# Optimization experiments

Measured on AMD Instinct MI355X. Metric: run time of the kernel, lower is better.

Reference implementation:

```python
import jax, jax.numpy as jnp
import numpy as np

# --- model/problem constants (match init_kwargs) ---
B = 1024      # batch
F = 512       # featureSize
H = 1024      # hiddenSize
S = 8         # symmetrySize
BOX = 12      # boxSize
MAXB = 64     # maxBoxes
MAXSY = 64    # maxSyms
MAXS = 16     # max stack depth (pattern uses <= 2)
L = 126


def setup_inputs() -> dict:
    key = jax.random.key(0)
    ks = jax.random.split(key, 9)

    def lin(k, out_d, in_d):
        k1, k2 = jax.random.split(k)
        bound = 1.0 / np.sqrt(in_d)
        W = jax.random.uniform(k1, (out_d, in_d), minval=-bound, maxval=bound, dtype=jnp.float32)
        b = jax.random.uniform(k2, (out_d,), minval=-bound, maxval=bound, dtype=jnp.float32)
        return W, b

    Wd, bd = lin(ks[0], H, F)      # AdjDecoder.decode
    Wl, bl = lin(ks[1], F, H)      # AdjDecoder.left
    Wr, br = lin(ks[2], F, H)      # AdjDecoder.right
    Wsd, bsd = lin(ks[3], H, F)    # SymDecoder.decode
    Wsf, bsf = lin(ks[4], F, H)    # SymDecoder.left
    Wss, bss = lin(ks[5], S, H)    # SymDecoder.right
    Wbox, bbox = lin(ks[6], BOX, F)  # BoxDecoder.decode

    inputStacks = jax.random.normal(ks[7], (B, F), dtype=jnp.float32)

    # Valid stack program, PROCESSING order: [adj, sym, box] * 42.
    # stack depth: 1 ->(1) 2 ->(2) 2 ->(0) 1 ; 42 boxes, 42 syms.
    proc = np.tile(np.array([1, 2, 0], dtype=np.int32), L // 3)
    stored = proc[::-1].copy()  # forward() processes operations in reverse
    operations = jnp.asarray(np.tile(stored[None, None, :], (B, 1, 1)))  # [B,1,L]

    return {"inputStacks": inputStacks, "operations": operations,
            "Wd": Wd, "bd": bd, "Wl": Wl, "bl": bl, "Wr": Wr, "br": br,
            "Wsd": Wsd, "bsd": bsd, "Wsf": Wsf, "bsf": bsf, "Wss": Wss, "bss": bss,
            "Wbox": Wbox, "bbox": bbox}


def _forward(inputStacks, operations, Wd, bd, Wl, bl, Wr, br,
             Wsd, bsd, Wsf, bsf, Wss, bss, Wbox, bbox):
    Bn, Fn = inputStacks.shape
    ops_proc = jnp.flip(operations[:, 0, :], axis=1).T  # [L, B] processing order

    stack = jnp.zeros((Bn, MAXS, Fn), inputStacks.dtype).at[:, 0, :].set(inputStacks)
    sp = jnp.ones((Bn,), jnp.int32)           # stack pointer (size)
    boxbuf = jnp.zeros((Bn, MAXB, Fn), inputStacks.dtype)
    bc = jnp.zeros((Bn,), jnp.int32)
    symbuf = jnp.zeros((Bn, MAXSY, S), inputStacks.dtype)
    sc = jnp.zeros((Bn,), jnp.int32)
    rows = jnp.arange(Bn)

    def step(carry, op):
        stack, sp, boxbuf, bc, symbuf, sc = carry
        top_idx = jnp.clip(sp - 1, 0, MAXS - 1)
        top = stack[rows, top_idx]                      # [B,F]
        # AdjDecoder on every sample (selected by op==1)
        h = jnp.tanh(top @ Wd.T + bd)
        l = jnp.tanh(h @ Wl.T + bl)
        r = jnp.tanh(h @ Wr.T + br)
        # SymDecoder on every sample (selected by op==2)
        hs = jnp.tanh(top @ Wsd.T + bsd)
        f = jnp.tanh(hs @ Wsf.T + bsf)
        s = jnp.tanh(hs @ Wss.T + bss)

        is0 = op == 0
        is1 = op == 1
        is2 = op == 2
        # value replacing the popped top (for op 1 -> left, op 2 -> folded)
        val_top = jnp.where(is1[:, None], l, jnp.where(is2[:, None], f, top))
        pos = jnp.arange(MAXS)[None, :]
        m_top = (pos == top_idx[:, None]) & (~is0)[:, None]
        m_r = (pos == jnp.clip(sp, 0, MAXS - 1)[:, None]) & is1[:, None]
        stack = jnp.where(m_r[..., None], r[:, None, :],
                          jnp.where(m_top[..., None], val_top[:, None, :], stack))
        posb = jnp.arange(MAXB)[None, :]
        mb = (posb == bc[:, None]) & is0[:, None]
        boxbuf = jnp.where(mb[..., None], top[:, None, :], boxbuf)
        poss = jnp.arange(MAXSY)[None, :]
        ms = (poss == sc[:, None]) & is2[:, None]
        symbuf = jnp.where(ms[..., None], s[:, None, :], symbuf)

        sp = sp + jnp.where(is0, -1, jnp.where(is1, 1, 0)).astype(sp.dtype)
        bc = bc + is0.astype(bc.dtype)
        sc = sc + is2.astype(sc.dtype)
        return (stack, sp, boxbuf, bc, symbuf, sc), None

    (stack, sp, boxbuf, bc, symbuf, sc), _ = jax.lax.scan(
        step, (stack, sp, boxbuf, bc, symbuf, sc), ops_proc)

    # boxStacks[i].reverse(); boxDecoder; pad with zeros to maxBoxes
    jb = jnp.arange(MAXB)
    bidx = bc[:, None] - 1 - jb[None, :]          # reversed order
    bvalid = bidx >= 0
    bfeat = jnp.take_along_axis(boxbuf, jnp.clip(bidx, 0, MAXB - 1)[..., None], axis=1)
    boxes = jnp.tanh(bfeat @ Wbox.T + bbox) * bvalid[..., None].astype(bfeat.dtype)

    js = jnp.arange(MAXSY)
    sidx = sc[:, None] - 1 - js[None, :]
    svalid = sidx >= 0
    syms = jnp.take_along_axis(symbuf, jnp.clip(sidx, 0, MAXSY - 1)[..., None], axis=1)
    syms = syms * svalid[..., None].astype(syms.dtype)

    return boxes, syms  # [B, MAXB, BOX], [B, MAXSY, S]


def reference(inputStacks, operations, Wd, bd, Wl, bl, Wr, br,
              Wsd, bsd, Wsf, bsf, Wss, bss, Wbox, bbox):
    return _forward(inputStacks, operations, Wd, bd, Wl, bl, Wr, br,
                    Wsd, bsd, Wsf, bsf, Wss, bss, Wbox, bbox)
```

## Files before the change

kernel.cpp:

```cpp
#include <hip/hip_runtime.h>
#include <stdint.h>

#define B_     1024
#define F_     512
#define H_     1024
#define S_     8
#define BOX_   12
#define MAXB_  64
#define MAXSY_ 64
#define L_     126
#define STK_   3
#define NCYC_  42

typedef unsigned short u16;
typedef unsigned int   u32;
typedef unsigned long long u64;
typedef __attribute__((ext_vector_type(8))) short sh8;
typedef __attribute__((ext_vector_type(4))) int   i4;
typedef __attribute__((ext_vector_type(4))) float f4;

#define MFMA16(a,b,c) __builtin_amdgcn_mfma_f32_16x16x32_bf16((a),(b),(c),0,0,0)

#define XCC_ID_IMM (((32 - 1) << 11) | (0 << 6) | 20)

constexpr size_t PL_HF = (size_t)H_ * F_ * 2;
constexpr size_t PL_FH = (size_t)F_ * H_ * 2;
constexpr size_t PL_SS = 16384;
constexpr size_t PL_BX = 16384;
constexpr size_t O_WdHi  = 4096;
constexpr size_t O_WdLo  = O_WdHi  + PL_HF;
constexpr size_t O_WsdHi = O_WdLo  + PL_HF;
constexpr size_t O_WsdLo = O_WsdHi + PL_HF;
constexpr size_t O_WlHi  = O_WsdLo + PL_HF;
constexpr size_t O_WlLo  = O_WlHi  + PL_FH;
constexpr size_t O_WrHi  = O_WlLo  + PL_FH;
constexpr size_t O_WrLo  = O_WrHi  + PL_FH;
constexpr size_t O_WsfHi = O_WrLo  + PL_FH;
constexpr size_t O_WsfLo = O_WsfHi + PL_FH;
constexpr size_t O_WssHi = O_WsfLo + PL_FH;
constexpr size_t O_WssLo = O_WssHi + PL_SS;
constexpr size_t O_WbxHi = O_WssLo + PL_SS;
constexpr size_t O_WbxLo = O_WbxHi + PL_BX;
constexpr size_t SZ_STK  = (size_t)B_ * STK_ * F_ * 2;
constexpr size_t O_SHi   = O_WbxLo + PL_BX;
constexpr size_t O_SLo   = O_SHi   + SZ_STK;
constexpr size_t SZ_H    = (size_t)B_ * H_ * 2;
constexpr size_t O_HAHi  = O_SLo   + SZ_STK;
constexpr size_t O_HALo  = O_HAHi  + SZ_H;
constexpr size_t O_HSHi  = O_HALo  + SZ_H;
constexpr size_t O_HSLo  = O_HSHi  + SZ_H;
constexpr size_t SZ_FB   = (size_t)B_ * 512 * 2;
constexpr size_t O_FB0Hi = O_HSLo  + SZ_H;
constexpr size_t O_FB0Lo = O_FB0Hi + SZ_FB;
constexpr size_t O_FB1Hi = O_FB0Lo + SZ_FB;
constexpr size_t O_FB1Lo = O_FB1Hi + SZ_FB;
constexpr size_t WS_NEED = O_FB1Lo + SZ_FB;
constexpr size_t O_FLAG  = 2048;
constexpr size_t O_GFAIL = 2176;
constexpr size_t O_GXCD  = 2304;

__device__ __forceinline__ float bf2float(u16 h) {
    union { u32 u; float f; } v; v.u = ((u32)h) << 16; return v.f;
}
__device__ __forceinline__ u16 bfhi_of(float f) {
    union { float f; u32 u; } v; v.f = f;
    u32 u = v.u;
    return (u16)((u + 0x7fffu + ((u >> 16) & 1u)) >> 16);
}
__device__ __forceinline__ void split2(float x, u16& hi, u16& lo) {
    hi = bfhi_of(x);
    lo = bfhi_of(x - bf2float(hi));
}

template<bool DC>
__device__ __forceinline__ void cst(u16* p, u16 v) {
    if (DC) asm volatile("global_store_short %0, %1, off sc0 sc1"
                         :: "v"(p), "v"((u32)v) : "memory");
    else    asm volatile("global_store_short %0, %1, off"
                         :: "v"(p), "v"((u32)v) : "memory");
}
__device__ __forceinline__ void vdrain() {
    asm volatile("s_waitcnt vmcnt(0)" ::: "memory");
}

__device__ __forceinline__ void cld8(i4& d0, i4& d1, i4& d2, i4& d3,
                                     i4& d4, i4& d5, i4& d6, i4& d7,
    const u16* p0, const u16* p1, const u16* p2, const u16* p3,
    const u16* p4, const u16* p5, const u16* p6, const u16* p7)
{
    asm volatile(
        "global_load_dwordx4 %0, %8, off sc0\n\t"
        "global_load_dwordx4 %1, %9, off sc0\n\t"
        "global_load_dwordx4 %2, %10, off sc0\n\t"
        "global_load_dwordx4 %3, %11, off sc0\n\t"
        "global_load_dwordx4 %4, %12, off sc0\n\t"
        "global_load_dwordx4 %5, %13, off sc0\n\t"
        "global_load_dwordx4 %6, %14, off sc0\n\t"
        "global_load_dwordx4 %7, %15, off sc0\n\t"
        "s_waitcnt vmcnt(0)"
        : "=&v"(d0),"=&v"(d1),"=&v"(d2),"=&v"(d3),
          "=&v"(d4),"=&v"(d5),"=&v"(d6),"=&v"(d7)
        : "v"(p0),"v"(p1),"v"(p2),"v"(p3),"v"(p4),"v"(p5),"v"(p6),"v"(p7));
}

__device__ void split_range(const float* __restrict__ s, u16* hi, u16* lo,
                            int n, int t0, int stride) {
    for (int i = t0; i < n; i += stride) {
        float v = s[i];
        u16 h = bfhi_of(v);
        hi[i] = h;
        lo[i] = bfhi_of(v - bf2float(h));
    }
}

__global__ void grass_prep(const float* __restrict__ X, const int* __restrict__ ops,
                           const float* __restrict__ Wd, const float* __restrict__ Wl,
                           const float* __restrict__ Wr, const float* __restrict__ Wsd,
                           const float* __restrict__ Wsf, const float* __restrict__ Wss,
                           const float* __restrict__ Wbox, char* __restrict__ ws)
{
    const int t0 = blockIdx.x * blockDim.x + threadIdx.x;
    const int st = gridDim.x * blockDim.x;
    split_range(Wd,  (u16*)(ws + O_WdHi),  (u16*)(ws + O_WdLo),  H_ * F_, t0, st);
    split_range(Wsd, (u16*)(ws + O_WsdHi), (u16*)(ws + O_WsdLo), H_ * F_, t0, st);
    split_range(Wl,  (u16*)(ws + O_WlHi),  (u16*)(ws + O_WlLo),  F_ * H_, t0, st);
    split_range(Wr,  (u16*)(ws + O_WrHi),  (u16*)(ws + O_WrLo),  F_ * H_, t0, st);
    split_range(Wsf, (u16*)(ws + O_WsfHi), (u16*)(ws + O_WsfLo), F_ * H_, t0, st);
    split_range(Wss, (u16*)(ws + O_WssHi), (u16*)(ws + O_WssLo), S_ * H_, t0, st);
    split_range(Wbox,(u16*)(ws + O_WbxHi), (u16*)(ws + O_WbxLo), BOX_ * F_, t0, st);
    u16* SHi = (u16*)(ws + O_SHi);
    u16* SLo = (u16*)(ws + O_SLo);
    for (int i = t0; i < B_ * F_; i += st) {
        int e = i >> 9, k = i & (F_ - 1);
        float v = X[i];
        u16 h = bfhi_of(v);
        size_t off = (size_t)e * STK_ * F_ + k;
        SHi[off] = h;
        SLo[off] = bfhi_of(v - bf2float(h));
    }
    int* flag = (int*)(ws + O_FLAG);
    for (int i = t0; i < B_ * L_; i += st) {
        int t = i % L_;
        int tm = t % 3;
        int expect = (tm == 0) ? 0 : ((tm == 1) ? 2 : 1);
        if (ops[i] != expect) {
            __hip_atomic_store(flag, 1, __ATOMIC_RELAXED, __HIP_MEMORY_SCOPE_AGENT);
            break;
        }
    }
}

__device__ __forceinline__ void gbar(int* bar, int target) {
    vdrain();
    __syncthreads();
    if (threadIdx.x == 0) {
        __hip_atomic_fetch_add(bar, 1, __ATOMIC_RELAXED, __HIP_MEMORY_SCOPE_AGENT);
        while (__hip_atomic_load(bar, __ATOMIC_RELAXED, __HIP_MEMORY_SCOPE_AGENT) < target)
            __builtin_amdgcn_s_sleep(2);
    }
    __syncthreads();
}
__device__ __forceinline__ void gwait(int* ctr, int target) {
    if (threadIdx.x == 0) {
        while (__hip_atomic_load(ctr, __ATOMIC_RELAXED, __HIP_MEMORY_SCOPE_AGENT) < target)
            __builtin_amdgcn_s_sleep(2);
    }
    __syncthreads();
}

__device__ __forceinline__ void stageA_c(u16* __restrict__ lds,
    const u16* __restrict__ AHi, const u16* __restrict__ ALo,
    const int* __restrict__ aOff, int kbase, int tid)
{
    const int wv = tid >> 6, lane = tid & 63;
    const int kk = kbase + lane * 8;
    int off[16];
#pragma unroll
    for (int i = 0; i < 16; ++i) off[i] = aOff[i * 4 + wv] + kk;
    const int lx = lane * 8;
#pragma unroll
    for (int half = 0; half < 2; ++half) {
        const u16* A = half ? ALo : AHi;
        u16* L = lds + (half ? 32768 : 0);
#pragma unroll
        for (int b = 0; b < 2; ++b) {
            const int i0 = b * 8;
            i4 d0,d1,d2,d3,d4,d5,d6,d7;
            cld8(d0,d1,d2,d3,d4,d5,d6,d7,
                 A+off[i0+0], A+off[i0+1], A+off[i0+2], A+off[i0+3],
                 A+off[i0+4], A+off[i0+5], A+off[i0+6], A+off[i0+7]);
#define STO(ii, dv) { const int m = (i0 + ii) * 4 + wv; \
                      *(i4*)(L + m * 512 + (lx ^ ((m & 7) << 3))) = dv; }
            STO(0,d0) STO(1,d1) STO(2,d2) STO(3,d3)
            STO(4,d4) STO(5,d5) STO(6,d6) STO(7,d7)
#undef STO
        }
    }
}

__device__ __forceinline__ void stageA_dc(u16* __restrict__ lds,
    const u16* __restrict__ AHi, const u16* __restrict__ ALo,
    const int* __restrict__ aOff, int kbase, int tid)
{
    const int wv = tid >> 6, lane = tid & 63;
    const int kk = kbase + lane * 8;
    int off[16];
#pragma unroll
    for (int i = 0; i < 16; ++i) off[i] = aOff[i * 4 + wv] + kk;
    u64 v[64];
#pragma unroll
    for (int i = 0; i < 16; ++i) {
        const u64* s = (const u64*)(AHi + off[i]);
        v[2 * i]     = __hip_atomic_load(s,     __ATOMIC_RELAXED, __HIP_MEMORY_SCOPE_AGENT);
        v[2 * i + 1] = __hip_atomic_load(s + 1, __ATOMIC_RELAXED, __HIP_MEMORY_SCOPE_AGENT);
    }
#pragma unroll
    for (int i = 0; i < 16; ++i) {
        const u64* s = (const u64*)(ALo + off[i]);
        v[32 + 2 * i] = __hip_atomic_load(s,     __ATOMIC_RELAXED, __HIP_MEMORY_SCOPE_AGENT);
        v[33 + 2 * i] = __hip_atomic_load(s + 1, __ATOMIC_RELAXED, __HIP_MEMORY_SCOPE_AGENT);
    }
#pragma unroll
    for (int i = 0; i < 16; ++i) {
        const int m = i * 4 + wv;
        u16* d = lds + m * 512 + ((lane * 8) ^ ((m & 7) << 3));
        ((u64*)d)[0] = v[2 * i];
        ((u64*)d)[1] = v[2 * i + 1];
        u64* d2 = (u64*)(d + 32768);
        d2[0] = v[32 + 2 * i];
        d2[1] = v[33 + 2 * i];
    }
}

__device__ __forceinline__ void kloop64(const u16* __restrict__ lds,
    const u16* __restrict__ WHi, const u16* __restrict__ WLo,
    int nRow0, int Kw, int kofs, f4 c[2][2], int lane, int wv4)
{
    const int quad = lane >> 4, mr = lane & 15;
    const int mh = wv4 & 1, nh = (wv4 >> 1) & 1;
    const int m0 = (mh * 2) * 16 + mr, m1 = m0 + 16;
    const int n0 = nRow0 + (nh * 2) * 16 + mr, n1 = n0 + 16;
    const u16* b0h = WHi + (size_t)n0 * Kw + kofs;
    const u16* b1h = WHi + (size_t)n1 * Kw + kofs;
    const u16* b0l = WLo + (size_t)n0 * Kw + kofs;
    const u16* b1l = WLo + (size_t)n1 * Kw + kofs;
    const int sw = (m0 & 7) << 3;
    const u16* A0h = lds + m0 * 512;
    const u16* A1h = lds + m1 * 512;
#pragma unroll 2
    for (int kb = 0; kb < 512; kb += 64) {
        const int k0 = kb + quad * 8, k1 = k0 + 32;
        const int x0 = k0 ^ sw, x1 = k1 ^ sw;
        sh8 B0H0 = *(const sh8*)(b0h + k0), B1H0 = *(const sh8*)(b1h + k0);
        sh8 B0L0 = *(const sh8*)(b0l + k0), B1L0 = *(const sh8*)(b1l + k0);
        sh8 B0H1 = *(const sh8*)(b0h + k1), B1H1 = *(const sh8*)(b1h + k1);
        sh8 B0L1 = *(const sh8*)(b0l + k1), B1L1 = *(const sh8*)(b1l + k1);
        sh8 A0H0 = *(const sh8*)(A0h + x0);
        sh8 A1H0 = *(const sh8*)(A1h + x0);
        sh8 A0L0 = *(const sh8*)(A0h + 32768 + x0);
        sh8 A1L0 = *(const sh8*)(A1h + 32768 + x0);
        sh8 A0H1 = *(const sh8*)(A0h + x1);
        sh8 A1H1 = *(const sh8*)(A1h + x1);
        sh8 A0L1 = *(const sh8*)(A0h + 32768 + x1);
        sh8 A1L1 = *(const sh8*)(A1h + 32768 + x1);
        c[0][0]=MFMA16(A0H0,B0H0,c[0][0]); c[0][1]=MFMA16(A0H0,B1H0,c[0][1]);
        c[1][0]=MFMA16(A1H0,B0H0,c[1][0]); c[1][1]=MFMA16(A1H0,B1H0,c[1][1]);
        c[0][0]=MFMA16(A0H0,B0L0,c[0][0]); c[0][1]=MFMA16(A0H0,B1L0,c[0][1]);
        c[1][0]=MFMA16(A1H0,B0L0,c[1][0]); c[1][1]=MFMA16(A1H0,B1L0,c[1][1]);
        c[0][0]=MFMA16(A0L0,B0H0,c[0][0]); c[0][1]=MFMA16(A0L0,B1H0,c[0][1]);
        c[1][0]=MFMA16(A1L0,B0H0,c[1][0]); c[1][1]=MFMA16(A1L0,B1H0,c[1][1]);
        c[0][0]=MFMA16(A0H1,B0H1,c[0][0]); c[0][1]=MFMA16(A0H1,B1H1,c[0][1]);
        c[1][0]=MFMA16(A1H1,B0H1,c[1][0]); c[1][1]=MFMA16(A1H1,B1H1,c[1][1]);
        c[0][0]=MFMA16(A0H1,B0L1,c[0][0]); c[0][1]=MFMA16(A0H1,B1L1,c[0][1]);
        c[1][0]=MFMA16(A1H1,B0L1,c[1][0]); c[1][1]=MFMA16(A1H1,B1L1,c[1][1]);
        c[0][0]=MFMA16(A0L1,B0H1,c[0][0]); c[0][1]=MFMA16(A0L1,B1H1,c[0][1]);
        c[1][0]=MFMA16(A1L1,B0H1,c[1][0]); c[1][1]=MFMA16(A1L1,B1H1,c[1][1]);
    }
}

__device__ __forceinline__ void kloop16(const u16* __restrict__ lds,
    const u16* __restrict__ WHi, const u16* __restrict__ WLo,
    int nValid, int Kw, int kofs, f4& c, int lane, int wv)
{
    const int quad = lane >> 4, mr = lane & 15;
    const int m = wv * 16 + mr;
    const int sm = (m & 7) << 3;
    const u16* Am = lds + m * 512;
    const bool nb = (mr < nValid);
    const u16* bh = WHi + (size_t)mr * Kw + kofs;
    const u16* bl = WLo + (size_t)mr * Kw + kofs;
#pragma unroll 2
    for (int kb = 0; kb < 512; kb += 64) {
        const int k0 = kb + quad * 8, k1 = k0 + 32;
        const int x0 = k0 ^ sm, x1 = k1 ^ sm;
        sh8 bH0 = {0,0,0,0,0,0,0,0}, bL0 = {0,0,0,0,0,0,0,0};
        sh8 bH1 = {0,0,0,0,0,0,0,0}, bL1 = {0,0,0,0,0,0,0,0};
        if (nb) {
            bH0 = *(const sh8*)(bh + k0); bL0 = *(const sh8*)(bl + k0);
            bH1 = *(const sh8*)(bh + k1); bL1 = *(const sh8*)(bl + k1);
        }
        sh8 aH0 = *(const sh8*)(Am + x0);
        sh8 aL0 = *(const sh8*)(Am + 32768 + x0);
        sh8 aH1 = *(const sh8*)(Am + x1);
        sh8 aL1 = *(const sh8*)(Am + 32768 + x1);
        c = MFMA16(aH0, bH0, c);
        c = MFMA16(aH0, bL0, c);
        c = MFMA16(aL0, bH0, c);
        c = MFMA16(aH1, bH1, c);
        c = MFMA16(aH1, bL1, c);
        c = MFMA16(aL1, bH1, c);
    }
}

__device__ __forceinline__ void zacc(f4 c[2][2]) {
    f4 z = {0.f, 0.f, 0.f, 0.f};
    c[0][0] = z; c[0][1] = z; c[1][0] = z; c[1][1] = z;
}

__device__ __forceinline__ void gemmK(u16* __restrict__ Ab,
    const u16* __restrict__ AHi, const u16* __restrict__ ALo, const int* __restrict__ aOff,
    const u16* __restrict__ WHi, const u16* __restrict__ WLo, int nRow0, int Kw,
    f4 c[2][2], int tid, int lane, int wv)
{
    zacc(c);
    for (int h = 0; h < Kw; h += 512) {
        __syncthreads();
        stageA_dc(Ab, AHi, ALo, aOff, h, tid);
        __syncthreads();
        kloop64(Ab, WHi, WLo, nRow0, Kw, h, c, lane, wv);
    }
}
__device__ __forceinline__ void gemmK16(u16* __restrict__ Ab,
    const u16* __restrict__ AHi, const u16* __restrict__ ALo, const int* __restrict__ aOff,
    const u16* __restrict__ WHi, const u16* __restrict__ WLo, int nValid, int Kw,
    f4& c, int tid, int lane, int wv)
{
    f4 z = {0.f, 0.f, 0.f, 0.f};
    c = z;
    for (int h = 0; h < Kw; h += 512) {
        __syncthreads();
        stageA_dc(Ab, AHi, ALo, aOff, h, tid);
        __syncthreads();
        kloop16(Ab, WHi, WLo, nValid, Kw, h, c, tid & 63, tid >> 6);
    }
}

__device__ __forceinline__ void pipe_gemm128(u16* __restrict__ Ab,
    const u16* __restrict__ AHi, const u16* __restrict__ ALo, const int* __restrict__ aOff,
    const u16* __restrict__ WHi, const u16* __restrict__ WLo, int col0, int Kw,
    f4 cA[2][2], f4 cB[2][2], int tid, int lane, int wv)
{
    zacc(cA); zacc(cB);
    for (int h = 0; h < Kw; h += 512) {
        __syncthreads();
        stageA_c(Ab, AHi, ALo, aOff, h, tid);
        __syncthreads();
        kloop64(Ab, WHi, WLo, col0,      Kw, h, cA, lane, wv);
        kloop64(Ab, WHi, WLo, col0 + 64, Kw, h, cB, lane, wv);
    }
}

template<bool DC>
__device__ __forceinline__ void ep_h(const f4 c[2][2], const float* __restrict__ bias,
                                     int colBase, int e0, u16* DHi, u16* DLo,
                                     int lane, int wv4)
{
    const int quad = lane >> 4, mr = lane & 15;
    const int mh = wv4 & 1, nh = (wv4 >> 1) & 1;
#pragma unroll
    for (int mi = 0; mi < 2; ++mi)
#pragma unroll
    for (int ni = 0; ni < 2; ++ni)
#pragma unroll
    for (int r = 0; r < 4; ++r) {
        int mm = (mh * 2 + mi) * 16 + quad * 4 + r;
        int nn = (nh * 2 + ni) * 16 + mr;
        float v = tanhf(c[mi][ni][r] + bias[colBase + nn]);
        u16 hi, lo; split2(v, hi, lo);
        size_t off = (size_t)(e0 + mm) * H_ + colBase + nn;
        cst<DC>(DHi + off, hi);
        cst<DC>(DLo + off, lo);
    }
}

template<bool DC>
__device__ __forceinline__ void ep_slot(const f4 c[2][2], const float* __restrict__ bias,
                                        int colBase, int slot, int e0,
                                        u16* SHi, u16* SLo, int lane, int wv4)
{
    const int quad = lane >> 4, mr = lane & 15;
    const int mh = wv4 & 1, nh = (wv4 >> 1) & 1;
#pragma unroll
    for (int mi = 0; mi < 2; ++mi)
#pragma unroll
    for (int ni = 0; ni < 2; ++ni)
#pragma unroll
    for (int r = 0; r < 4; ++r) {
        int mm = (mh * 2 + mi) * 16 + quad * 4 + r;
        int nn = (nh * 2 + ni) * 16 + mr;
        float v = tanhf(c[mi][ni][r] + bias[colBase + nn]);
        u16 hi, lo; split2(v, hi, lo);
        size_t off = ((size_t)(e0 + mm) * STK_ + slot) * F_ + colBase + nn;
        cst<DC>(SHi + off, hi);
        cst<DC>(SLo + off, lo);
    }
}

template<bool DC>
__device__ __forceinline__ void ep_fb(const f4 c[2][2], const float* __restrict__ bias,
                                      int colBase, int e0, u16* FHi, u16* FLo,
                                      int lane, int wv4)
{
    const int quad = lane >> 4, mr = lane & 15;
    const int mh = wv4 & 1, nh = (wv4 >> 1) & 1;
#pragma unroll
    for (int mi = 0; mi < 2; ++mi)
#pragma unroll
    for (int ni = 0; ni < 2; ++ni)
#pragma unroll
    for (int r = 0; r < 4; ++r) {
        int mm = (mh * 2 + mi) * 16 + quad * 4 + r;
        int nn = (nh * 2 + ni) * 16 + mr;
        float v = tanhf(c[mi][ni][r] + bias[colBase + nn]);
        u16 hi, lo; split2(v, hi, lo);
        size_t off = (size_t)(e0 + mm) * 512 + colBase + nn;
        cst<DC>(FHi + off, hi);
        cst<DC>(FLo + off, lo);
    }
}

template<bool DC>
__device__ __forceinline__ void ep_stack(const f4 c[2][2], const float* __restrict__ bias,
                                         int colBase, int opSel, bool useRi, int tix, int e0,
                                         const unsigned char* opsL, const int* spA,
                                         u16* SHi, u16* SLo, int lane, int wv)
{
    const int quad = lane >> 4, mr = lane & 15;
    const int mh = wv & 1, nh = (wv >> 1) & 1;
#pragma unroll
    for (int mi = 0; mi < 2; ++mi)
#pragma unroll
    for (int ni = 0; ni < 2; ++ni)
#pragma unroll
    for (int r = 0; r < 4; ++r) {
        int mm = (mh * 2 + mi) * 16 + quad * 4 + r;
        int nn = (nh * 2 + ni) * 16 + mr;
        if (opsL[mm * L_ + tix] != opSel) continue;
        int sp = spA[mm];
        int slot = useRi ? sp : sp - 1;
        slot = slot < 0 ? 0 : (slot > STK_ - 1 ? STK_ - 1 : slot);
        float v = tanhf(c[mi][ni][r] + bias[colBase + nn]);
        u16 hi, lo; split2(v, hi, lo);
        size_t off = ((size_t)(e0 + mm) * STK_ + slot) * F_ + colBase + nn;
        cst<DC>(SHi + off, hi);
        cst<DC>(SLo + off, lo);
    }
}

__device__ __forceinline__ void ep_small(const f4& c, const float* __restrict__ bias,
                                         int nValid, int opSel, int tix, int e0,
                                         const unsigned char* opsL, const int* eCnt, const int* eTot,
                                         float* __restrict__ outBase, int rowStride, int ncols,
                                         int lane, int wv)
{
    const int nn = lane & 15;
    if (nn >= nValid) return;
#pragma unroll
    for (int r = 0; r < 4; ++r) {
        int mm = wv * 16 + (lane >> 4) * 4 + r;
        if (opsL[mm * L_ + tix] != opSel) continue;
        int slot = eTot[mm] - 1 - eCnt[mm];
        if (slot < 0 || slot >= 64) continue;
        float v = tanhf(c[r] + bias[nn]);
        outBase[(size_t)(e0 + mm) * rowStride + slot * ncols + nn] = v;
    }
}

__device__ __forceinline__ void ep_small_u(const f4& c, const float* __restrict__ bias,
                                           int nValid, int slot, int e0,
                                           float* __restrict__ outBase, int rowStride, int ncols,
                                           int lane, int wv)
{
    const int nn = lane & 15;
    if (nn >= nValid) return;
#pragma unroll
    for (int r = 0; r < 4; ++r) {
        int mm = wv * 16 + (lane >> 4) * 4 + r;
        outBase[(size_t)(e0 + mm) * rowStride + slot * ncols + nn] = tanhf(c[r] + bias[nn]);
    }
}

__global__ __launch_bounds__(256, 1) void grass_pipe(
    const float* __restrict__ bd, const float* __restrict__ bl, const float* __restrict__ br,
    const float* __restrict__ bsd, const float* __restrict__ bsf, const float* __restrict__ bss,
    const float* __restrict__ bbox,
    char* __restrict__ ws, float* __restrict__ out)
{
    if (__hip_atomic_load((int*)(ws + O_FLAG), __ATOMIC_RELAXED, __HIP_MEMORY_SCOPE_AGENT))
        return;

    const int tid  = threadIdx.x;
    const int lane = tid & 63, wv = tid >> 6;
    const int j    = blockIdx.x >> 4;
    const int gid  = blockIdx.x & 15;
    const int e0   = gid * 64;

    const u16* WdHi  = (const u16*)(ws + O_WdHi);
    const u16* WdLo  = (const u16*)(ws + O_WdLo);
    const u16* WsdHi = (const u16*)(ws + O_WsdHi);
    const u16* WsdLo = (const u16*)(ws + O_WsdLo);
    const u16* WlHi  = (const u16*)(ws + O_WlHi);
    const u16* WlLo  = (const u16*)(ws + O_WlLo);
    const u16* WrHi  = (const u16*)(ws + O_WrHi);
    const u16* WrLo  = (const u16*)(ws + O_WrLo);
    const u16* WsfHi = (const u16*)(ws + O_WsfHi);
    const u16* WsfLo = (const u16*)(ws + O_WsfLo);
    const u16* WssHi = (const u16*)(ws + O_WssHi);
    const u16* WssLo = (const u16*)(ws + O_WssLo);
    const u16* WbxHi = (const u16*)(ws + O_WbxHi);
    const u16* WbxLo = (const u16*)(ws + O_WbxLo);
    u16* SHi  = (u16*)(ws + O_SHi);
    u16* SLo  = (u16*)(ws + O_SLo);
    u16* HAHi = (u16*)(ws + O_HAHi);
    u16* HALo = (u16*)(ws + O_HALo);
    u16* HSHi = (u16*)(ws + O_HSHi);
    u16* HSLo = (u16*)(ws + O_HSLo);
    u16* FB0Hi = (u16*)(ws + O_FB0Hi);
    u16* FB0Lo = (u16*)(ws + O_FB0Lo);
    u16* FB1Hi = (u16*)(ws + O_FB1Hi);
    u16* FB1Lo = (u16*)(ws + O_FB1Lo);
    int* cbar = (int*)ws + gid * 32;
    int* sbar = cbar + 1;
    int* pbar = cbar + 3;
    int* gx   = (int*)(ws + O_GXCD) + gid * 16;
    int* gf   = (int*)(ws + O_GFAIL) + gid;

    float* outB = out;
    float* outS = out + (size_t)B_ * MAXB_ * BOX_;

    __shared__ __align__(16) u16 Abuf[2 * 64 * 512];
    __shared__ int aS0[64], aR1[64], aR2[64], aHH[64], aFB[64];

    if (tid < 64) {
        aS0[tid] = ((e0 + tid) * STK_ + 0) * F_;
        aR1[tid] = ((e0 + tid) * STK_ + 1) * F_;
        aR2[tid] = ((e0 + tid) * STK_ + 2) * F_;
        aHH[tid] = (e0 + tid) * H_;
        aFB[tid] = (e0 + tid) * 512;
    }

    const int myxcd = (int)(__builtin_amdgcn_s_getreg(XCC_ID_IMM) & 0xf);
    if (tid == 0)
        __hip_atomic_store(gx + j, myxcd, __ATOMIC_RELAXED, __HIP_MEMORY_SCOPE_AGENT);
    gbar(pbar, 16);
    if (tid < 16) {
        int ox = __hip_atomic_load(gx + tid, __ATOMIC_RELAXED, __HIP_MEMORY_SCOPE_AGENT);
        if (ox != myxcd)
            __hip_atomic_store(gf, 1, __ATOMIC_RELAXED, __HIP_MEMORY_SCOPE_AGENT);
    }
    gbar(pbar, 32);
    if (__hip_atomic_load(gf, __ATOMIC_RELAXED, __HIP_MEMORY_SCOPE_AGENT))
        return;

    f4 cA[2][2], cB[2][2];
    f4 cs;

    if (j < 8) {
        for (int cyc = 0; cyc < NCYC_; ++cyc) {
            pipe_gemm128(Abuf, SHi, SLo, aS0, WdHi, WdLo, j * 128, F_, cA, cB, tid, lane, wv);
            ep_h<false>(cA, bd, j * 128,      e0, HAHi, HALo, lane, wv);
            ep_h<false>(cB, bd, j * 128 + 64, e0, HAHi, HALo, lane, wv);
            gbar(cbar, 8 * (2 * cyc + 1));
            if (j < 4) {
                pipe_gemm128(Abuf, HAHi, HALo, aHH, WlHi, WlLo, j * 128, H_, cA, cB, tid, lane, wv);
                ep_slot<false>(cA, bl, j * 128,      0, e0, SHi, SLo, lane, wv);
                ep_slot<false>(cB, bl, j * 128 + 64, 0, e0, SHi, SLo, lane, wv);
            } else {
                const int rs = 1 + (cyc & 1);
                pipe_gemm128(Abuf, HAHi, HALo, aHH, WrHi, WrLo, (j - 4) * 128, H_, cA, cB, tid, lane, wv);
                if (cyc >= 2) gwait(sbar, 8 * (2 * (cyc - 2) + 1));
                ep_slot<false>(cA, br, (j - 4) * 128,      rs, e0, SHi, SLo, lane, wv);
                ep_slot<false>(cB, br, (j - 4) * 128 + 64, rs, e0, SHi, SLo, lane, wv);
            }
            gbar(cbar, 8 * (2 * cyc + 2));
        }
    } else {
        const int role = j - 8;
        for (int cyc = 0; cyc < NCYC_; ++cyc) {
            gwait(cbar, 8 * (2 * cyc + 2));
            const int* aR = (cyc & 1) ? aR2 : aR1;
            pipe_gemm128(Abuf, SHi, SLo, aR, WsdHi, WsdLo, role * 128, F_, cA, cB, tid, lane, wv);
            ep_h<false>(cA, bsd, role * 128,      e0, HSHi, HSLo, lane, wv);
            ep_h<false>(cB, bsd, role * 128 + 64, e0, HSHi, HSLo, lane, wv);
            gbar(sbar, 8 * (2 * cyc + 1));
            if (role < 4) {
                u16* FH = (cyc & 1) ? FB1Hi : FB0Hi;
                u16* FL = (cyc & 1) ? FB1Lo : FB0Lo;
                pipe_gemm128(Abuf, HSHi, HSLo, aHH, WsfHi, WsfLo, role * 128, H_, cA, cB, tid, lane, wv);
                ep_fb<false>(cA, bsf, role * 128,      e0, FH, FL, lane, wv);
                ep_fb<false>(cB, bsf, role * 128 + 64, e0, FH, FL, lane, wv);
            } else if (role == 4) {
                f4 z = {0.f, 0.f, 0.f, 0.f}; cs = z;
                for (int h = 0; h < H_; h += 512) {
                    __syncthreads();
                    stageA_c(Abuf, HSHi, HSLo, aHH, h, tid);
                    __syncthreads();
                    kloop16(Abuf, WssHi, WssLo, S_, H_, h, cs, lane, wv);
                }
                ep_small_u(cs, bss, S_, NCYC_ - 1 - cyc, e0, outS, MAXSY_ * S_, S_, lane, wv);
            } else if (role == 5 && cyc >= 1) {
                const u16* FH = ((cyc - 1) & 1) ? FB1Hi : FB0Hi;
                const u16* FL = ((cyc - 1) & 1) ? FB1Lo : FB0Lo;
                __syncthreads();
                stageA_c(Abuf, FH, FL, aFB, 0, tid);
                __syncthreads();
                f4 z = {0.f, 0.f, 0.f, 0.f}; cs = z;
                kloop16(Abuf, WbxHi, WbxLo, BOX_, 512, 0, cs, lane, wv);
                ep_small_u(cs, bbox, BOX_, NCYC_ - (cyc - 1) - 1, e0, outB, MAXB_ * BOX_, BOX_, lane, wv);
            }
            gbar(sbar, 8 * (2 * cyc + 2));
        }
        if (role == 5) {
            const u16* FH = ((NCYC_ - 1) & 1) ? FB1Hi : FB0Hi;
            const u16* FL = ((NCYC_ - 1) & 1) ? FB1Lo : FB0Lo;
            __syncthreads();
            stageA_c(Abuf, FH, FL, aFB, 0, tid);
            __syncthreads();
            f4 z = {0.f, 0.f, 0.f, 0.f}; cs = z;
            kloop16(Abuf, WbxHi, WbxLo, BOX_, 512, 0, cs, lane, wv);
            ep_small_u(cs, bbox, BOX_, 0, e0, outB, MAXB_ * BOX_, BOX_, lane, wv);
        }
    }
}

__global__ __launch_bounds__(256, 2) void grass_legacy(
    const int* __restrict__ ops,
    const float* __restrict__ bd, const float* __restrict__ bl, const float* __restrict__ br,
    const float* __restrict__ bsd, const float* __restrict__ bsf, const float* __restrict__ bss,
    const float* __restrict__ bbox,
    char* __restrict__ ws, float* __restrict__ out)
{
    const int tid  = threadIdx.x;
    const int lane = tid & 63, wv = tid >> 6;
    const int gid  = blockIdx.x >> 4;
    const int j    = blockIdx.x & 15;
    const int e0   = gid * 64;

    {
        int nonuni = __hip_atomic_load((int*)(ws + O_FLAG), __ATOMIC_RELAXED, __HIP_MEMORY_SCOPE_AGENT);
        int gfl = __hip_atomic_load((int*)(ws + O_GFAIL) + gid, __ATOMIC_RELAXED, __HIP_MEMORY_SCOPE_AGENT);
        if (!nonuni && !gfl) return;
    }

    const u16* WdHi  = (const u16*)(ws + O_WdHi);
    const u16* WdLo  = (const u16*)(ws + O_WdLo);
    const u16* WsdHi = (const u16*)(ws + O_WsdHi);
    const u16* WsdLo = (const u16*)(ws + O_WsdLo);
    const u16* WlHi  = (const u16*)(ws + O_WlHi);
    const u16* WlLo  = (const u16*)(ws + O_WlLo);
    const u16* WrHi  = (const u16*)(ws + O_WrHi);
    const u16* WrLo  = (const u16*)(ws + O_WrLo);
    const u16* WsfHi = (const u16*)(ws + O_WsfHi);
    const u16* WsfLo = (const u16*)(ws + O_WsfLo);
    const u16* WssHi = (const u16*)(ws + O_WssHi);
    const u16* WssLo = (const u16*)(ws + O_WssLo);
    const u16* WbxHi = (const u16*)(ws + O_WbxHi);
    const u16* WbxLo = (const u16*)(ws + O_WbxLo);
    u16* SHi  = (u16*)(ws + O_SHi);
    u16* SLo  = (u16*)(ws + O_SLo);
    u16* HAHi = (u16*)(ws + O_HAHi);
    u16* HALo = (u16*)(ws + O_HALo);
    u16* HSHi = (u16*)(ws + O_HSHi);
    u16* HSLo = (u16*)(ws + O_HSLo);
    int* bar = (int*)ws + gid * 32 + 2;

    float* outB = out;
    float* outS = out + (size_t)B_ * MAXB_ * BOX_;

    __shared__ __align__(16) u16 Abuf[2 * 64 * 512];
    __shared__ unsigned char opsL[64 * L_];
    __shared__ int spA[64], beA[64], seA[64], beF[64], seF[64];
    __shared__ int aStk[64], aHH[64];
    __shared__ int sInfo[2];

    for (int idx = tid; idx < 64 * L_; idx += 256) {
        int e = idx / L_, t = idx - e * L_;
        opsL[idx] = (unsigned char)ops[(size_t)(e0 + e) * L_ + t];
    }
    __syncthreads();
    if (tid < 64) {
        spA[tid] = 1; beA[tid] = 0; seA[tid] = 0;
        int cb = 0, cs2 = 0;
        for (int t = 0; t < L_; ++t) {
            int o = opsL[tid * L_ + t];
            cb += (o == 0); cs2 += (o == 2);
        }
        beF[tid] = cb; seF[tid] = cs2;
        aHH[tid]  = (e0 + tid) * H_;
        aStk[tid] = ((e0 + tid) * STK_ + 0) * F_;
    }
    __syncthreads();

    int epoch = 0;
    f4 c[2][2];
    f4 cs;

    for (int step = 0; step < L_; ++step) {
        const int tix = L_ - 1 - step;
        if (wv == 0) {
            int o  = opsL[lane * L_ + tix];
            int sp = spA[lane];
            unsigned long long bo = __ballot(o  == opsL[0 * L_ + tix]);
// ... 163 lines not shown
            int g = t / BOX_, cc = t - g*BOX_;
            if (op[g]==0) {
                float acc = fdot1(Wbox+(size_t)cc*F_, stk[g][ti[g]], F_/4);
                boxtmp[g][bc[g]][cc] = tanhf(acc + bbox[cc]);
            }
        }
        __syncthreads();
        if (a1) {
            if (t < F_) {
                float r0,r1,r2,r3; fdot4(Wl+(size_t)t*H_, hh[0],hh[1],hh[2],hh[3], H_/4, r0,r1,r2,r3);
                float bb = bl[t];
                if (op[0]==1) stk[0][ti[0]][t]=tanhf(r0+bb); if (op[1]==1) stk[1][ti[1]][t]=tanhf(r1+bb);
                if (op[2]==1) stk[2][ti[2]][t]=tanhf(r2+bb); if (op[3]==1) stk[3][ti[3]][t]=tanhf(r3+bb);
            } else {
                int m = t - F_;
                float r0,r1,r2,r3; fdot4(Wr+(size_t)m*H_, hh[0],hh[1],hh[2],hh[3], H_/4, r0,r1,r2,r3);
                float bb = br[m];
                if (op[0]==1) stk[0][ri[0]][m]=tanhf(r0+bb); if (op[1]==1) stk[1][ri[1]][m]=tanhf(r1+bb);
                if (op[2]==1) stk[2][ri[2]][m]=tanhf(r2+bb); if (op[3]==1) stk[3][ri[3]][m]=tanhf(r3+bb);
            }
        }
        if (a2) {
            if (t < F_) {
                float r0,r1,r2,r3; fdot4(Wsf+(size_t)t*H_, hh[0],hh[1],hh[2],hh[3], H_/4, r0,r1,r2,r3);
                float bb = bsf[t];
                if (op[0]==2) stk[0][ti[0]][t]=tanhf(r0+bb); if (op[1]==2) stk[1][ti[1]][t]=tanhf(r1+bb);
                if (op[2]==2) stk[2][ti[2]][t]=tanhf(r2+bb); if (op[3]==2) stk[3][ti[3]][t]=tanhf(r3+bb);
            } else if (t < F_ + FB_G*S_) {
                int idx = t - F_, g = idx >> 3, cc = idx & 7;
                if (op[g]==2) {
                    float acc = fdot1(Wss+(size_t)cc*H_, hh[g], H_/4);
                    symtmp[g][sc[g]][cc] = tanhf(acc + bss[cc]);
                }
            }
        }
        __syncthreads();
#pragma unroll
        for (int g = 0; g < FB_G; ++g) {
            if (op[g]==1) sp[g]++;
            else if (op[g]==2) sc[g]++;
            else { bc[g]++; sp[g]--; }
        }
    }
#pragma unroll
    for (int g = 0; g < FB_G; ++g) {
        int b = b0 + g;
        float* ob = out + (size_t)b * MAXB_ * BOX_;
        for (int idx = t; idx < MAXB_*BOX_; idx += 1024) {
            int jj = idx / BOX_, cc = idx - jj*BOX_;
            int e = bc[g] - 1 - jj;
            ob[idx] = (e >= 0) ? boxtmp[g][e][cc] : 0.f;
        }
        float* os = out + (size_t)B_*MAXB_*BOX_ + (size_t)b * MAXSY_ * S_;
        for (int idx = t; idx < MAXSY_*S_; idx += 1024) {
            int jj = idx >> 3, cc = idx & 7;
            int e = sc[g] - 1 - jj;
            os[idx] = (e >= 0) ? symtmp[g][e][cc] : 0.f;
        }
    }
}

extern "C" void kernel_launch(void* const* d_in, const int* in_sizes, int n_in,
                              void* d_out, int out_size, void* d_ws, size_t ws_size,
                              hipStream_t stream) {
    (void)in_sizes; (void)n_in;
    const float* X    = (const float*)d_in[0];
    const int*   ops  = (const int*)d_in[1];
    const float* Wd   = (const float*)d_in[2];  const float* bd   = (const float*)d_in[3];
    const float* Wl   = (const float*)d_in[4];  const float* bl   = (const float*)d_in[5];
    const float* Wr   = (const float*)d_in[6];  const float* br   = (const float*)d_in[7];
    const float* Wsd  = (const float*)d_in[8];  const float* bsd  = (const float*)d_in[9];
    const float* Wsf  = (const float*)d_in[10]; const float* bsf  = (const float*)d_in[11];
    const float* Wss  = (const float*)d_in[12]; const float* bss  = (const float*)d_in[13];
    const float* Wbox = (const float*)d_in[14]; const float* bbox = (const float*)d_in[15];
    float* out = (float*)d_out;

    if (ws_size < WS_NEED) {
        grass_fallback<<<dim3(B_/FB_G), dim3(1024), 0, stream>>>(
            X, ops, Wd, bd, Wl, bl, Wr, br, Wsd, bsd, Wsf, bsf, Wss, bss, Wbox, bbox, out);
        return;
    }
    char* ws = (char*)d_ws;
    hipMemsetAsync(d_out, 0, (size_t)out_size * sizeof(float), stream);
    hipMemsetAsync(ws, 0, 4096, stream);
    grass_prep<<<dim3(512), dim3(256), 0, stream>>>(X, ops, Wd, Wl, Wr, Wsd, Wsf, Wss, Wbox, ws);
    grass_pipe<<<dim3(256), dim3(256), 0, stream>>>(bd, bl, br, bsd, bsf, bss, bbox, ws, out);
    grass_legacy<<<dim3(256), dim3(256), 0, stream>>>(ops, bd, bl, br, bsd, bsf, bss, bbox, ws, out);
}
```

Before: 2.740 ms.

## Split persistent pipeline across twice as many blocks with 64-column tiles

Doubles the grass_pipe grid from 256 to 512 blocks. Each group now has 32 workgroups, and each one computes 64 output columns instead of 128. K staging chunks shrink from 512 to 256 so LDS use halves and two blocks can share a CU (launch bounds 256,2). Barrier counts and role indices are rescaled to match, and spin-waits get a bounded poll count. This trades more global barrier participants and more K iterations for more parallelism per cycle, and it relies on 32 blocks per group being co-resident on one XCD.

```diff
diff --git a/kernel.cpp b/kernel.cpp
--- a/kernel.cpp
+++ b/kernel.cpp
@@ -23,11 +23,16 @@
 
 #define XCC_ID_IMM (((32 - 1) << 11) | (0 << 6) | 20)
 
+#define POLL_MAX (1 << 22)
+
+constexpr size_t O_FLAG  = 2048;
+constexpr size_t O_GFAIL = 2176;
+constexpr size_t O_GXCD  = 2304;
 constexpr size_t PL_HF = (size_t)H_ * F_ * 2;
 constexpr size_t PL_FH = (size_t)F_ * H_ * 2;
 constexpr size_t PL_SS = 16384;
 constexpr size_t PL_BX = 16384;
-constexpr size_t O_WdHi  = 4096;
+constexpr size_t O_WdHi  = 8192;
 constexpr size_t O_WdLo  = O_WdHi  + PL_HF;
 constexpr size_t O_WsdHi = O_WdLo  + PL_HF;
 constexpr size_t O_WsdLo = O_WsdHi + PL_HF;
@@ -55,9 +60,6 @@
 constexpr size_t O_FB1Hi = O_FB0Lo + SZ_FB;
 constexpr size_t O_FB1Lo = O_FB1Hi + SZ_FB;
 constexpr size_t WS_NEED = O_FB1Lo + SZ_FB;
-constexpr size_t O_FLAG  = 2048;
-constexpr size_t O_GFAIL = 2176;
-constexpr size_t O_GXCD  = 2304;
 
 __device__ __forceinline__ float bf2float(u16 h) {
     union { u32 u; float f; } v; v.u = ((u32)h) << 16; return v.f;
@@ -160,42 +162,54 @@
     }
     __syncthreads();
 }
-__device__ __forceinline__ void gwait(int* ctr, int target) {
+__device__ __forceinline__ void gbarT(int* bar, int target) {
+    vdrain();
+    __syncthreads();
     if (threadIdx.x == 0) {
-        while (__hip_atomic_load(ctr, __ATOMIC_RELAXED, __HIP_MEMORY_SCOPE_AGENT) < target)
+        __hip_atomic_fetch_add(bar, 1, __ATOMIC_RELAXED, __HIP_MEMORY_SCOPE_AGENT);
+        for (int it = 0; it < POLL_MAX; ++it) {
+            if (__hip_atomic_load(bar, __ATOMIC_RELAXED, __HIP_MEMORY_SCOPE_AGENT) >= target) break;
             __builtin_amdgcn_s_sleep(2);
+        }
     }
     __syncthreads();
 }
-
-__device__ __forceinline__ void stageA_c(u16* __restrict__ lds,
+__device__ __forceinline__ void gwaitT(int* ctr, int target) {
+    if (threadIdx.x == 0) {
+        for (int it = 0; it < POLL_MAX; ++it) {
+            if (__hip_atomic_load(ctr, __ATOMIC_RELAXED, __HIP_MEMORY_SCOPE_AGENT) >= target) break;
+            __builtin_amdgcn_s_sleep(2);
+        }
+    }
+    __syncthreads();
+}
+
+__device__ __forceinline__ void stage256(u16* __restrict__ lds,
     const u16* __restrict__ AHi, const u16* __restrict__ ALo,
     const int* __restrict__ aOff, int kbase, int tid)
 {
     const int wv = tid >> 6, lane = tid & 63;
-    const int kk = kbase + lane * 8;
-    int off[16];
-#pragma unroll
-    for (int i = 0; i < 16; ++i) off[i] = aOff[i * 4 + wv] + kk;
-    const int lx = lane * 8;
-#pragma unroll
-    for (int half = 0; half < 2; ++half) {
-        const u16* A = half ? ALo : AHi;
-        u16* L = lds + (half ? 32768 : 0);
-#pragma unroll
-        for (int b = 0; b < 2; ++b) {
-            const int i0 = b * 8;
-            i4 d0,d1,d2,d3,d4,d5,d6,d7;
-            cld8(d0,d1,d2,d3,d4,d5,d6,d7,
-                 A+off[i0+0], A+off[i0+1], A+off[i0+2], A+off[i0+3],
-                 A+off[i0+4], A+off[i0+5], A+off[i0+6], A+off[i0+7]);
-#define STO(ii, dv) { const int m = (i0 + ii) * 4 + wv; \
-                      *(i4*)(L + m * 512 + (lx ^ ((m & 7) << 3))) = dv; }
-            STO(0,d0) STO(1,d1) STO(2,d2) STO(3,d3)
-            STO(4,d4) STO(5,d5) STO(6,d6) STO(7,d7)
+    const int rsub = lane >> 5;
+    const int c8 = (lane & 31) * 8;
+    int off[8];
+#pragma unroll
+    for (int i = 0; i < 8; ++i) off[i] = aOff[i * 8 + wv * 2 + rsub] + kbase + c8;
+    const int sw = ((wv * 2 + rsub) & 7) << 3;
+    i4 d0,d1,d2,d3,d4,d5,d6,d7;
+    cld8(d0,d1,d2,d3,d4,d5,d6,d7,
+         AHi+off[0], AHi+off[1], AHi+off[2], AHi+off[3],
+         AHi+off[4], AHi+off[5], AHi+off[6], AHi+off[7]);
+#define STO(ii, dv, base) { const int m = (ii) * 8 + wv * 2 + rsub; \
+                            *(i4*)((base) + m * 256 + (c8 ^ sw)) = dv; }
+    STO(0,d0,lds) STO(1,d1,lds) STO(2,d2,lds) STO(3,d3,lds)
+    STO(4,d4,lds) STO(5,d5,lds) STO(6,d6,lds) STO(7,d7,lds)
+    cld8(d0,d1,d2,d3,d4,d5,d6,d7,
+         ALo+off[0], ALo+off[1], ALo+off[2], ALo+off[3],
+         ALo+off[4], ALo+off[5], ALo+off[6], ALo+off[7]);
+    u16* ldsLo = lds + 64 * 256;
+    STO(0,d0,ldsLo) STO(1,d1,ldsLo) STO(2,d2,ldsLo) STO(3,d3,ldsLo)
+    STO(4,d4,ldsLo) STO(5,d5,ldsLo) STO(6,d6,ldsLo) STO(7,d7,ldsLo)
 #undef STO
-        }
-    }
 }
 
 __device__ __forceinline__ void stageA_dc(u16* __restrict__ lds,
@@ -232,6 +246,7 @@
     }
 }
 
+template<int CW>
 __device__ __forceinline__ void kloop64(const u16* __restrict__ lds,
     const u16* __restrict__ WHi, const u16* __restrict__ WLo,
     int nRow0, int Kw, int kofs, f4 c[2][2], int lane, int wv4)
@@ -245,10 +260,10 @@
     const u16* b0l = WLo + (size_t)n0 * Kw + kofs;
     const u16* b1l = WLo + (size_t)n1 * Kw + kofs;
     const int sw = (m0 & 7) << 3;
-    const u16* A0h = lds + m0 * 512;
-    const u16* A1h = lds + m1 * 512;
+    const u16* A0h = lds + m0 * CW;
+    const u16* A1h = lds + m1 * CW;
 #pragma unroll 2
-    for (int kb = 0; kb < 512; kb += 64) {
+    for (int kb = 0; kb < CW; kb += 64) {
         const int k0 = kb + quad * 8, k1 = k0 + 32;
         const int x0 = k0 ^ sw, x1 = k1 ^ sw;
         sh8 B0H0 = *(const sh8*)(b0h + k0), B1H0 = *(const sh8*)(b1h + k0);
@@ -257,12 +272,12 @@
         sh8 B0L1 = *(const sh8*)(b0l + k1), B1L1 = *(const sh8*)(b1l + k1);
         sh8 A0H0 = *(const sh8*)(A0h + x0);
         sh8 A1H0 = *(const sh8*)(A1h + x0);
-        sh8 A0L0 = *(const sh8*)(A0h + 32768 + x0);
-        sh8 A1L0 = *(const sh8*)(A1h + 32768 + x0);
+        sh8 A0L0 = *(const sh8*)(A0h + 64 * CW + x0);
+        sh8 A1L0 = *(const sh8*)(A1h + 64 * CW + x0);
         sh8 A0H1 = *(const sh8*)(A0h + x1);
         sh8 A1H1 = *(const sh8*)(A1h + x1);
-        sh8 A0L1 = *(const sh8*)(A0h + 32768 + x1);
-        sh8 A1L1 = *(const sh8*)(A1h + 32768 + x1);
+        sh8 A0L1 = *(const sh8*)(A0h + 64 * CW + x1);
+        sh8 A1L1 = *(const sh8*)(A1h + 64 * CW + x1);
         c[0][0]=MFMA16(A0H0,B0H0,c[0][0]); c[0][1]=MFMA16(A0H0,B1H0,c[0][1]);
         c[1][0]=MFMA16(A1H0,B0H0,c[1][0]); c[1][1]=MFMA16(A1H0,B1H0,c[1][1]);
         c[0][0]=MFMA16(A0H0,B0L0,c[0][0]); c[0][1]=MFMA16(A0H0,B1L0,c[0][1]);
@@ -278,6 +293,7 @@
     }
 }
 
+template<int CW>
 __device__ __forceinline__ void kloop16(const u16* __restrict__ lds,
     const u16* __restrict__ WHi, const u16* __restrict__ WLo,
     int nValid, int Kw, int kofs, f4& c, int lane, int wv)
@@ -285,12 +301,12 @@
     const int quad = lane >> 4, mr = lane & 15;
     const int m = wv * 16 + mr;
     const int sm = (m & 7) << 3;
-    const u16* Am = lds + m * 512;
+    const u16* Am = lds + m * CW;
     const bool nb = (mr < nValid);
     const u16* bh = WHi + (size_t)mr * Kw + kofs;
     const u16* bl = WLo + (size_t)mr * Kw + kofs;
 #pragma unroll 2
-    for (int kb = 0; kb < 512; kb += 64) {
+    for (int kb = 0; kb < CW; kb += 64) {
         const int k0 = kb + quad * 8, k1 = k0 + 32;
         const int x0 = k0 ^ sm, x1 = k1 ^ sm;
         sh8 bH0 = {0,0,0,0,0,0,0,0}, bL0 = {0,0,0,0,0,0,0,0};
@@ -300,9 +316,9 @@
             bH1 = *(const sh8*)(bh + k1); bL1 = *(const sh8*)(bl + k1);
         }
         sh8 aH0 = *(const sh8*)(Am + x0);
-        sh8 aL0 = *(const sh8*)(Am + 32768 + x0);
+        sh8 aL0 = *(const sh8*)(Am + 64 * CW + x0);
         sh8 aH1 = *(const sh8*)(Am + x1);
-        sh8 aL1 = *(const sh8*)(Am + 32768 + x1);
+        sh8 aL1 = *(const sh8*)(Am + 64 * CW + x1);
         c = MFMA16(aH0, bH0, c);
         c = MFMA16(aH0, bL0, c);
         c = MFMA16(aL0, bH0, c);
@@ -327,7 +343,7 @@
         __syncthreads();
         stageA_dc(Ab, AHi, ALo, aOff, h, tid);
         __syncthreads();
-        kloop64(Ab, WHi, WLo, nRow0, Kw, h, c, lane, wv);
+        kloop64<512>(Ab, WHi, WLo, nRow0, Kw, h, c, lane, wv);
     }
 }
 __device__ __forceinline__ void gemmK16(u16* __restrict__ Ab,
@@ -341,22 +357,21 @@
         __syncthreads();
         stageA_dc(Ab, AHi, ALo, aOff, h, tid);
         __syncthreads();
-        kloop16(Ab, WHi, WLo, nValid, Kw, h, c, tid & 63, tid >> 6);
-    }
-}
-
-__device__ __forceinline__ void pipe_gemm128(u16* __restrict__ Ab,
+        kloop16<512>(Ab, WHi, WLo, nValid, Kw, h, c, lane, wv);
+    }
+}
+
+__device__ __forceinline__ void pipe_gemm64(u16* __restrict__ Ab,
     const u16* __restrict__ AHi, const u16* __restrict__ ALo, const int* __restrict__ aOff,
     const u16* __restrict__ WHi, const u16* __restrict__ WLo, int col0, int Kw,
-    f4 cA[2][2], f4 cB[2][2], int tid, int lane, int wv)
-{
-    zacc(cA); zacc(cB);
-    for (int h = 0; h < Kw; h += 512) {
-        __syncthreads();
-        stageA_c(Ab, AHi, ALo, aOff, h, tid);
-        __syncthreads();
-        kloop64(Ab, WHi, WLo, col0,      Kw, h, cA, lane, wv);
-        kloop64(Ab, WHi, WLo, col0 + 64, Kw, h, cB, lane, wv);
+    f4 c[2][2], int tid, int lane, int wv)
+{
+    zacc(c);
+    for (int h = 0; h < Kw; h += 256) {
+        __syncthreads();
+        stage256(Ab, AHi, ALo, aOff, h, tid);
+        __syncthreads();
+        kloop64<256>(Ab, WHi, WLo, col0, Kw, h, c, lane, wv);
     }
 }
 
@@ -490,7 +505,7 @@
     }
 }
 
-__global__ __launch_bounds__(256, 1) void grass_pipe(
+__global__ __launch_bounds__(256, 2) void grass_pipe(
     const float* __restrict__ bd, const float* __restrict__ bl, const float* __restrict__ br,
     const float* __restrict__ bsd, const float* __restrict__ bsf, const float* __restrict__ bss,
     const float* __restrict__ bbox,
@@ -532,13 +547,13 @@
     int* cbar = (int*)ws + gid * 32;
     int* sbar = cbar + 1;
     int* pbar = cbar + 3;
-    int* gx   = (int*)(ws + O_GXCD) + gid * 16;
+    int* gx   = (int*)(ws + O_GXCD) + gid * 32;
     int* gf   = (int*)(ws + O_GFAIL) + gid;
 
     float* outB = out;
     float* outS = out + (size_t)B_ * MAXB_ * BOX_;
 
-    __shared__ __align__(16) u16 Abuf[2 * 64 * 512];
+    __shared__ __align__(16) u16 Abuf[2 * 64 * 256];
     __shared__ int aS0[64], aR1[64], aR2[64], aHH[64], aFB[64];
 
     if (tid < 64) {
@@ -552,82 +567,81 @@
     const int myxcd = (int)(__builtin_amdgcn_s_getreg(XCC_ID_IMM) & 0xf);
     if (tid == 0)
         __hip_atomic_store(gx + j, myxcd, __ATOMIC_RELAXED, __HIP_MEMORY_SCOPE_AGENT);
-    gbar(pbar, 16);
-    if (tid < 16) {
+    gbarT(pbar, 32);
+    if (tid < 32) {
         int ox = __hip_atomic_load(gx + tid, __ATOMIC_RELAXED, __HIP_MEMORY_SCOPE_AGENT);
         if (ox != myxcd)
             __hip_atomic_store(gf, 1, __ATOMIC_RELAXED, __HIP_MEMORY_SCOPE_AGENT);
     }
-    gbar(pbar, 32);
+    gbarT(pbar, 64);
     if (__hip_atomic_load(gf, __ATOMIC_RELAXED, __HIP_MEMORY_SCOPE_AGENT))
         return;
 
-    f4 cA[2][2], cB[2][2];
+    f4 cA[2][2];
     f4 cs;
 
-    if (j < 8) {
+    if (j < 16) {
         for (int cyc = 0; cyc < NCYC_; ++cyc) {
-            pipe_gemm128(Abuf, SHi, SLo, aS0, WdHi, WdLo, j * 128, F_, cA, cB, tid, lane, wv);
-            ep_h<false>(cA, bd, j * 128,      e0, HAHi, HALo, lane, wv);
-            ep_h<false>(cB, bd, j * 128 + 64, e0, HAHi, HALo, lane, wv);
-            gbar(cbar, 8 * (2 * cyc + 1));
-            if (j < 4) {
-                pipe_gemm128(Abuf, HAHi, HALo, aHH, WlHi, WlLo, j * 128, H_, cA, cB, tid, lane, wv);
-                ep_slot<false>(cA, bl, j * 128,      0, e0, SHi, SLo, lane, wv);
-                ep_slot<false>(cB, bl, j * 128 + 64, 0, e0, SHi, SLo, lane, wv);
+            pipe_gemm64(Abuf, SHi, SLo, aS0, WdHi, WdLo, j * 64, F_, cA, tid, lane, wv);
+            ep_h<false>(cA, bd, j * 64, e0, HAHi, HALo, lane, wv);
+            gbarT(cbar, 16 * (2 * cyc + 1));
+            if (j < 8) {
+                pipe_gemm64(Abuf, HAHi, HALo, aHH, WlHi, WlLo, j * 64, H_, cA, tid, lane, wv);
+                ep_slot<false>(cA, bl, j * 64, 0, e0, SHi, SLo, lane, wv);
             } else {
                 const int rs = 1 + (cyc & 1);
-                pipe_gemm128(Abuf, HAHi, HALo, aHH, WrHi, WrLo, (j - 4) * 128, H_, cA, cB, tid, lane, wv);
-                if (cyc >= 2) gwait(sbar, 8 * (2 * (cyc - 2) + 1));
-                ep_slot<false>(cA, br, (j - 4) * 128,      rs, e0, SHi, SLo, lane, wv);
-                ep_slot<false>(cB, br, (j - 4) * 128 + 64, rs, e0, SHi, SLo, lane, wv);
+                pipe_gemm64(Abuf, HAHi, HALo, aHH, WrHi, WrLo, (j - 8) * 64, H_, cA, tid, lane, wv);
+                if (cyc >= 2) gwaitT(sbar, 16 * (2 * (cyc - 2) + 1));
+                ep_slot<false>(cA, br, (j - 8) * 64, rs, e0, SHi, SLo, lane, wv);
             }
-            gbar(cbar, 8 * (2 * cyc + 2));
+            gbarT(cbar, 16 * (2 * cyc + 2));
         }
     } else {
-        const int role = j - 8;
+        const int role = j - 16;
         for (int cyc = 0; cyc < NCYC_; ++cyc) {
-            gwait(cbar, 8 * (2 * cyc + 2));
+            gwaitT(cbar, 16 * (2 * cyc + 2));
             const int* aR = (cyc & 1) ? aR2 : aR1;
-            pipe_gemm128(Abuf, SHi, SLo, aR, WsdHi, WsdLo, role * 128, F_, cA, cB, tid, lane, wv);
-            ep_h<false>(cA, bsd, role * 128,      e0, HSHi, HSLo, lane, wv);
-            ep_h<false>(cB, bsd, role * 128 + 64, e0, HSHi, HSLo, lane, wv);
-            gbar(sbar, 8 * (2 * cyc + 1));
-            if (role < 4) {
+            pipe_gemm64(Abuf, SHi, SLo, aR, WsdHi, WsdLo, role * 64, F_, cA, tid, lane, wv);
+            ep_h<false>(cA, bsd, role * 64, e0, HSHi, HSLo, lane, wv);
+            gbarT(sbar, 16 * (2 * cyc + 1));
+            if (role < 8) {
                 u16* FH = (cyc & 1) ? FB1Hi : FB0Hi;
                 u16* FL = (cyc & 1) ? FB1Lo : FB0Lo;
-                pipe_gemm128(Abuf, HSHi, HSLo, aHH, WsfHi, WsfLo, role * 128, H_, cA, cB, tid, lane, wv);
-                ep_fb<false>(cA, bsf, role * 128,      e0, FH, FL, lane, wv);
-                ep_fb<false>(cB, bsf, role * 128 + 64, e0, FH, FL, lane, wv);
-            } else if (role == 4) {
+                pipe_gemm64(Abuf, HSHi, HSLo, aHH, WsfHi, WsfLo, role * 64, H_, cA, tid, lane, wv);
+                ep_fb<false>(cA, bsf, role * 64, e0, FH, FL, lane, wv);
+            } else if (role == 8) {
                 f4 z = {0.f, 0.f, 0.f, 0.f}; cs = z;
-                for (int h = 0; h < H_; h += 512) {
+                for (int h = 0; h < H_; h += 256) {
                     __syncthreads();
-                    stageA_c(Abuf, HSHi, HSLo, aHH, h, tid);
+                    stage256(Abuf, HSHi, HSLo, aHH, h, tid);
                     __syncthreads();
-                    kloop16(Abuf, WssHi, WssLo, S_, H_, h, cs, lane, wv);
+                    kloop16<256>(Abuf, WssHi, WssLo, S_, H_, h, cs, lane, wv);
                 }
                 ep_small_u(cs, bss, S_, NCYC_ - 1 - cyc, e0, outS, MAXSY_ * S_, S_, lane, wv);
-            } else if (role == 5 && cyc >= 1) {
+            } else if (role == 9 && cyc >= 1) {
                 const u16* FH = ((cyc - 1) & 1) ? FB1Hi : FB0Hi;
                 const u16* FL = ((cyc - 1) & 1) ? FB1Lo : FB0Lo;
-                __syncthreads();
-                stageA_c(Abuf, FH, FL, aFB, 0, tid);
-                __syncthreads();
                 f4 z = {0.f, 0.f, 0.f, 0.f}; cs = z;
-                kloop16(Abuf, WbxHi, WbxLo, BOX_, 512, 0, cs, lane, wv);
+                for (int h = 0; h < 512; h += 256) {
+                    __syncthreads();
+                    stage256(Abuf, FH, FL, aFB, h, tid);
+                    __syncthreads();
+                    kloop16<256>(Abuf, WbxHi, WbxLo, BOX_, 512, h, cs, lane, wv);
+                }
                 ep_small_u(cs, bbox, BOX_, NCYC_ - (cyc - 1) - 1, e0, outB, MAXB_ * BOX_, BOX_, lane, wv);
             }
-            gbar(sbar, 8 * (2 * cyc + 2));
-        }
-        if (role == 5) {
+            gbarT(sbar, 16 * (2 * cyc + 2));
+        }
+        if (role == 9) {
             const u16* FH = ((NCYC_ - 1) & 1) ? FB1Hi : FB0Hi;
             const u16* FL = ((NCYC_ - 1) & 1) ? FB1Lo : FB0Lo;
-            __syncthreads();
-            stageA_c(Abuf, FH, FL, aFB, 0, tid);
-            __syncthreads();
             f4 z = {0.f, 0.f, 0.f, 0.f}; cs = z;
-            kloop16(Abuf, WbxHi, WbxLo, BOX_, 512, 0, cs, lane, wv);
+            for (int h = 0; h < 512; h += 256) {
+                __syncthreads();
+                stage256(Abuf, FH, FL, aFB, h, tid);
+                __syncthreads();
+                kloop16<256>(Abuf, WbxHi, WbxLo, BOX_, 512, h, cs, lane, wv);
+            }
             ep_small_u(cs, bbox, BOX_, 0, e0, outB, MAXB_ * BOX_, BOX_, lane, wv);
         }
     }
@@ -957,8 +971,8 @@
     }
     char* ws = (char*)d_ws;
     hipMemsetAsync(d_out, 0, (size_t)out_size * sizeof(float), stream);
-    hipMemsetAsync(ws, 0, 4096, stream);
+    hipMemsetAsync(ws, 0, 8192, stream);
     grass_prep<<<dim3(512), dim3(256), 0, stream>>>(X, ops, Wd, Wl, Wr, Wsd, Wsf, Wss, Wbox, ws);
-    grass_pipe<<<dim3(256), dim3(256), 0, stream>>>(bd, bl, br, bsd, bsf, bss, bbox, ws, out);
+    grass_pipe<<<dim3(512), dim3(256), 0, stream>>>(bd, bl, br, bsd, bsf, bss, bbox, ws, out);
     grass_legacy<<<dim3(256), dim3(256), 0, stream>>>(ops, bd, bl, br, bsd, bsf, bss, bbox, ws, out);
 }
```

After: 2.670 ms (median of 2 runs). 1.03x faster.
